# Kernel optimization log

Measured on AMD Instinct MI355X. Metric: run time of the kernel, lower is better.

The kernel has to match this reference:

```python
import jax, jax.numpy as jnp
import numpy as np

D_MODEL = 1024
NHEAD = 16
HEAD_DIM = D_MODEL // NHEAD
WINDOW = 256


def setup_inputs() -> dict:
    key = jax.random.key(0)
    kx, kq, kk, kv, ko = jax.random.split(key, 5)
    B, S = 2, 2048
    scale = 1.0 / np.sqrt(D_MODEL)
    x = jax.random.normal(kx, (B, S, D_MODEL), dtype=jnp.float32)
    Wq = jax.random.normal(kq, (D_MODEL, D_MODEL), dtype=jnp.float32) * scale
    Wk = jax.random.normal(kk, (D_MODEL, D_MODEL), dtype=jnp.float32) * scale
    Wv = jax.random.normal(kv, (D_MODEL, D_MODEL), dtype=jnp.float32) * scale
    Wo = jax.random.normal(ko, (D_MODEL, D_MODEL), dtype=jnp.float32) * scale
    return {"x": x, "Wq": Wq, "Wk": Wk, "Wv": Wv, "Wo": Wo}


def _sliding_window_mask(seq_len):
    # additive mask: 0 where (q - window + 1) <= k <= q, -inf elsewhere
    pos = jnp.arange(seq_len)
    qpos = pos[:, None]
    kpos = pos[None, :]
    valid = (kpos >= qpos - WINDOW + 1) & (kpos <= qpos)
    return jnp.where(valid, 0.0, -jnp.inf).astype(jnp.float32)


def reference(x, Wq, Wk, Wv, Wo):
    B, S, D = x.shape
    # projections (nn.Linear: x @ W.T; weights here stored as [out,in] equiv -> use x @ W.T)
    q = jnp.einsum('bsd,ed->bse', x, Wq)
    k = jnp.einsum('bsd,ed->bse', x, Wk)
    v = jnp.einsum('bsd,ed->bse', x, Wv)
    q = q.reshape(B, S, NHEAD, HEAD_DIM).transpose(0, 2, 1, 3)  # [B,H,S,Dh]
    k = k.reshape(B, S, NHEAD, HEAD_DIM).transpose(0, 2, 1, 3)
    v = v.reshape(B, S, NHEAD, HEAD_DIM).transpose(0, 2, 1, 3)
    mask = _sliding_window_mask(S)  # [S,S]
    scale = 1.0 / np.sqrt(HEAD_DIM)
    scores = jnp.einsum('bhqd,bhkd->bhqk', q, k) * scale + mask
    attn = jax.nn.softmax(scores, axis=-1)
    out = jnp.einsum('bhqk,bhkd->bhqd', attn, v)  # [B,H,S,Dh]
    out = out.transpose(0, 2, 1, 3).reshape(B, S, D)
    return jnp.einsum('bsd,ed->bse', out, Wo)
```

## Files before the change

kernel.cpp:

```cpp
#include <hip/hip_runtime.h>
#include <stdint.h>

#define S_LEN   2048
#define BATCH   2
#define DM      1024
#define NHEADS  16
#define HD      64
#define WIN     256
#define MROWS   (BATCH * S_LEN)
#define NX      (MROWS * DM)
#define NW      (DM * DM)

typedef unsigned short u16;
typedef unsigned int   u32;

using short8  = __attribute__((ext_vector_type(8))) short;
using floatx4 = __attribute__((ext_vector_type(4))) float;

__device__ __forceinline__ float bf2f(u16 u) {
    union { u32 u; float f; } v; v.u = ((u32)u) << 16; return v.f;
}
__device__ __forceinline__ u16 f2bf(float f) {
    union { float f; u32 u; } v; v.f = f;
    u32 u = v.u;
    u += 0x7fffu + ((u >> 16) & 1u);
    return (u16)(u >> 16);
}

__device__ __forceinline__ void load_lds16(const void* g, void* l) {
    __builtin_amdgcn_global_load_lds(
        (__attribute__((address_space(1))) void*)(uintptr_t)g,
        (__attribute__((address_space(3))) void*)(unsigned int)(uintptr_t)l,
        16, 0, 0);
}

__global__ __launch_bounds__(256) void detect_mode(const u16* x, int* flag) {
    __shared__ int sbad;
    int t = threadIdx.x;
    if (t == 0) sbad = 0;
    __syncthreads();
    int bad = 0;
    for (int i = t; i < 4096; i += 256) {
        float v = bf2f(x[i]);
        if (!(fabsf(v) < 1e6f)) bad = 1;
    }
    if (bad) atomicOr(&sbad, 1);
    __syncthreads();
    if (t == 0) flag[0] = sbad;
}

__global__ __launch_bounds__(256) void normalize_inputs(
        const void* x, const void* wq, const void* wk, const void* wv, const void* wo,
        u16* xb, u16* wcat, u16* wob, const int* flag) {
    if (flag[0] == 0) return;
    const int total = NX + 4 * NW;
    for (int i = blockIdx.x * blockDim.x + threadIdx.x; i < total;
         i += gridDim.x * blockDim.x) {
        const void* src; u16* dst; int li;
        if (i < NX)              { src = x;  dst = xb;            li = i; }
        else if (i < NX + NW)    { src = wq; dst = wcat;          li = i - NX; }
        else if (i < NX + 2*NW)  { src = wk; dst = wcat + NW;     li = i - NX - NW; }
        else if (i < NX + 3*NW)  { src = wv; dst = wcat + 2*NW;   li = i - NX - 2*NW; }
        else                     { src = wo; dst = wob;           li = i - NX - 3*NW; }
        dst[li] = f2bf(((const float*)src)[li]);
    }
}

#define BM 128
#define BK 32

template<int TBN>
__global__ __launch_bounds__(256) void gemm_lds(
        const u16* __restrict__ Araw, const u16* __restrict__ Anorm,
        const u16* __restrict__ B0, const u16* __restrict__ B1,
        const u16* __restrict__ B2, const u16* __restrict__ Bnorm,
        void* __restrict__ C, int M, int N, int K,
        const int* __restrict__ flag, int final_out) {
    constexpr int NF = TBN / 32;
    __shared__ __align__(16) u16 sA[2][BM * BK];
    __shared__ __align__(16) u16 sB[2][TBN * BK];

    const int mode = flag[0];
    const int tid  = threadIdx.x;
    const int lane = tid & 63, wave = tid >> 6;
    const int m0  = blockIdx.x * BM;
    const int n0g = blockIdx.y * TBN;
    const int third = n0g >> 10;
    const u16* A = mode ? Anorm : Araw;
    const u16* B = mode ? (Bnorm + (size_t)third * NW)
                        : (third == 0 ? B0 : (third == 1 ? B1 : B2));
    const int n0 = n0g - third * 1024;

    const int srow = lane >> 2;
    const int scol = (lane & 3) * 8;
    const u16* gA = A + (size_t)(m0 + wave * 16 + srow) * K + scol;
    const u16* gB = B + (size_t)(n0 + wave * 16 + srow) * K + scol;
    const size_t rstep = (size_t)64 * K;
    const int lofs = wave * 16 * BK;

    const int n16 = lane & 15, quad = lane >> 4;
    const int m_off = (wave >> 1) * 64, n_off = (wave & 1) * (TBN / 2);

    floatx4 acc[4][NF] = {};
    const int NIT = K / BK;

    auto issue = [&](int k0, int buf) {
        u16* lA = sA[buf] + lofs;
        u16* lB = sB[buf] + lofs;
        load_lds16(gA + k0,         lA);
        load_lds16(gA + k0 + rstep, lA + 64 * BK);
        load_lds16(gB + k0, lB);
        if (TBN == 128) load_lds16(gB + k0 + rstep, lB + 64 * BK);
    };

    issue(0, 0);
    for (int it = 0; it < NIT; ++it) {
        const int cur = it & 1;
        __syncthreads();
        if (it + 1 < NIT) issue((it + 1) * BK, 1 - cur);
        short8 af[4], bfr[NF];
        #pragma unroll
        for (int i = 0; i < 4; ++i)
            af[i] = *(const short8*)&sA[cur][(m_off + i * 16 + n16) * BK + quad * 8];
        #pragma unroll
        for (int j = 0; j < NF; ++j)
            bfr[j] = *(const short8*)&sB[cur][(n_off + j * 16 + n16) * BK + quad * 8];
        #pragma unroll
        for (int i = 0; i < 4; ++i) {
            #pragma unroll
            for (int j = 0; j < NF; ++j)
                acc[i][j] = __builtin_amdgcn_mfma_f32_16x16x32_bf16(
                    af[i], bfr[j], acc[i][j], 0, 0, 0);
        }
    }

    const int outmode = final_out ? mode : 0;
    const float oscale = (!final_out && n0g < 1024) ? 0.125f : 1.0f;
    #pragma unroll
    for (int i = 0; i < 4; ++i) {
        #pragma unroll
        for (int j = 0; j < NF; ++j) {
            #pragma unroll
            for (int r = 0; r < 4; ++r) {
                int row = m0 + m_off + i * 16 + quad * 4 + r;
                int col = n0g + n_off + j * 16 + n16;
                size_t idx = (size_t)row * N + col;
                float v = acc[i][j][r] * oscale;
                if (outmode) ((float*)C)[idx] = v;
                else         ((u16*)C)[idx]   = f2bf(v);
            }
        }
    }
}

#define NCHUNK 10

__global__ __launch_bounds__(256) void attn_mfma(
        const u16* __restrict__ QKV, u16* __restrict__ O) {
    __shared__ __align__(16) u16 sK[2][32][72];
    __shared__ __align__(16) u16 sVt[2][64][40];
    __shared__ __align__(16) u16 sP[4][2][16][40];

    const int bh = blockIdx.x;
    const int b  = bh >> 4, h = bh & 15;
    const int q0 = blockIdx.y * 64;
    const int kb0 = q0 - (WIN - 1);
    const int tid = threadIdx.x;
    const u16* base = QKV + (size_t)b * S_LEN * 3072;
    const u16* Kb = base + 1024 + h * 64;
    const u16* Vb = base + 2048 + h * 64;

    const int srow = tid >> 3;
    const int sseg = tid & 7;

    auto stage = [&](int c, int buf) {
        int kg = kb0 + c * 32 + srow;
        uint4 kv = {0u, 0u, 0u, 0u}, vv = {0u, 0u, 0u, 0u};
        if (kg >= 0 && kg < S_LEN) {
            kv = *(const uint4*)(Kb + (size_t)kg * 3072 + sseg * 8);
            vv = *(const uint4*)(Vb + (size_t)kg * 3072 + sseg * 8);
        }
        *(uint4*)&sK[buf][srow][sseg * 8] = kv;
        const u16* vp = (const u16*)&vv;
        #pragma unroll
        for (int t2 = 0; t2 < 8; ++t2) sVt[buf][sseg * 8 + t2][srow] = vp[t2];
    };

    const int wave = tid >> 6, lane = tid & 63;
    const int n16 = lane & 15, quad = lane >> 4;
    const int sqb = q0 + wave * 16;
    const int sq_r0 = sqb + quad * 4;
    const int cfirst = wave >> 1;

    const u16* qrow = base + (size_t)(sqb + n16) * 3072 + h * 64;
    short8 aq0 = *(const short8*)(qrow + quad * 8);
    short8 aq1 = *(const short8*)(qrow + 32 + quad * 8);

    floatx4 o0 = {0.f,0.f,0.f,0.f}, o1 = o0, o2 = o0, o3 = o0;
    float m[4] = {-1e30f, -1e30f, -1e30f, -1e30f};
    float l[4] = {0.f, 0.f, 0.f, 0.f};

    stage(0, 0);
    for (int c = 0; c < NCHUNK; ++c) {
        const int buf = c & 1;
        __syncthreads();
        if (c + 1 < NCHUNK) stage(c + 1, 1 - buf);
        if (c < cfirst || c > cfirst + 8) continue;

        short8 bk00 = *(const short8*)&sK[buf][n16][quad * 8];
        short8 bk01 = *(const short8*)&sK[buf][n16][32 + quad * 8];
        short8 bk10 = *(const short8*)&sK[buf][16 + n16][quad * 8];
        short8 bk11 = *(const short8*)&sK[buf][16 + n16][32 + quad * 8];
        floatx4 z = {0.f, 0.f, 0.f, 0.f};
        floatx4 s0 = __builtin_amdgcn_mfma_f32_16x16x32_bf16(aq0, bk00, z, 0, 0, 0);
        s0 = __builtin_amdgcn_mfma_f32_16x16x32_bf16(aq1, bk01, s0, 0, 0, 0);
        floatx4 s1 = __builtin_amdgcn_mfma_f32_16x16x32_bf16(aq0, bk10, z, 0, 0, 0);
        s1 = __builtin_amdgcn_mfma_f32_16x16x32_bf16(aq1, bk11, s1, 0, 0, 0);

        const int kg0 = kb0 + c * 32 + n16;
        const int kg1 = kg0 + 16;
        float alpha[4], p0[4], p1[4];
        #pragma unroll
        for (int r = 0; r < 4; ++r) {
            int sq = sq_r0 + r;
            int lo = sq - (WIN - 1); if (lo < 0) lo = 0;
            float v0 = (kg0 >= lo && kg0 <= sq) ? s0[r] : -1e30f;
            float v1 = (kg1 >= lo && kg1 <= sq) ? s1[r] : -1e30f;
            float mc = fmaxf(v0, v1);
            mc = fmaxf(mc, __shfl_xor(mc, 1));
            mc = fmaxf(mc, __shfl_xor(mc, 2));
            mc = fmaxf(mc, __shfl_xor(mc, 4));
            mc = fmaxf(mc, __shfl_xor(mc, 8));
            float mn = fmaxf(m[r], mc);
            alpha[r] = __expf(m[r] - mn);
            m[r] = mn;
            p0[r] = __expf(v0 - mn);
            p1[r] = __expf(v1 - mn);
            float rs = p0[r] + p1[r];
            rs += __shfl_xor(rs, 1);
            rs += __shfl_xor(rs, 2);
            rs += __shfl_xor(rs, 4);
            rs += __shfl_xor(rs, 8);
            l[r] = l[r] * alpha[r] + rs;
        }
        #pragma unroll
        for (int r = 0; r < 4; ++r) {
            o0[r] *= alpha[r]; o1[r] *= alpha[r];
            o2[r] *= alpha[r]; o3[r] *= alpha[r];
        }
        u16* pw = &sP[wave][c & 1][0][0];
        #pragma unroll
        for (int r = 0; r < 4; ++r) {
            pw[(quad * 4 + r) * 40 + n16]      = f2bf(p0[r]);
            pw[(quad * 4 + r) * 40 + 16 + n16] = f2bf(p1[r]);
        }
        asm volatile("s_waitcnt lgkmcnt(0)" ::: "memory");
        short8 pa  = *(const short8*)&pw[n16 * 40 + quad * 8];
        short8 bv0 = *(const short8*)&sVt[buf][n16]     [quad * 8];
        short8 bv1 = *(const short8*)&sVt[buf][16 + n16][quad * 8];
        short8 bv2 = *(const short8*)&sVt[buf][32 + n16][quad * 8];
        short8 bv3 = *(const short8*)&sVt[buf][48 + n16][quad * 8];
        o0 = __builtin_amdgcn_mfma_f32_16x16x32_bf16(pa, bv0, o0, 0, 0, 0);
        o1 = __builtin_amdgcn_mfma_f32_16x16x32_bf16(pa, bv1, o1, 0, 0, 0);
        o2 = __builtin_amdgcn_mfma_f32_16x16x32_bf16(pa, bv2, o2, 0, 0, 0);
        o3 = __builtin_amdgcn_mfma_f32_16x16x32_bf16(pa, bv3, o3, 0, 0, 0);
    }

    #pragma unroll
    for (int r = 0; r < 4; ++r) {
        float rl = 1.0f / l[r];
        size_t ro = ((size_t)(b * S_LEN + sq_r0 + r)) * DM + h * 64 + n16;
        O[ro]      = f2bf(o0[r] * rl);
        O[ro + 16] = f2bf(o1[r] * rl);
        O[ro + 32] = f2bf(o2[r] * rl);
        O[ro + 48] = f2bf(o3[r] * rl);
    }
}

extern "C" void kernel_launch(void* const* d_in, const int* in_sizes, int n_in,
                              void* d_out, int out_size, void* d_ws, size_t ws_size,
                              hipStream_t stream) {
    char* ws = (char*)d_ws;
    int* flag = (int*)ws;
    u16* xb   = (u16*)(ws + 1024);
    u16* wcat = xb   + (size_t)NX;
    u16* wob  = wcat + (size_t)3 * NW;
    u16* qkv  = wob  + (size_t)NW;
    u16* ob   = qkv  + (size_t)MROWS * 3 * DM;

    const u16* xr  = (const u16*)d_in[0];
    const u16* wqr = (const u16*)d_in[1];
    const u16* wkr = (const u16*)d_in[2];
    const u16* wvr = (const u16*)d_in[3];
    const u16* wor = (const u16*)d_in[4];

    detect_mode<<<1, 256, 0, stream>>>(xr, flag);
    normalize_inputs<<<1024, 256, 0, stream>>>(
        d_in[0], d_in[1], d_in[2], d_in[3], d_in[4], xb, wcat, wob, flag);
    gemm_lds<128><<<dim3(MROWS / BM, 3072 / 128), 256, 0, stream>>>(
        xr, xb, wqr, wkr, wvr, wcat, qkv, MROWS, 3 * DM, DM, flag, 0);
    attn_mfma<<<dim3(BATCH * NHEADS, S_LEN / 64), 256, 0, stream>>>(qkv, ob);
    gemm_lds<64><<<dim3(MROWS / BM, DM / 64), 256, 0, stream>>>(
        ob, ob, wor, wor, wor, wob, d_out, MROWS, DM, DM, flag, 1);
}
```

Measured before the change: 178.9 us.

## Pre-transpose V into a head-major buffer and fold mode detection into normalize

A new transpose_v kernel writes V as [b,h,d,s] into an extra workspace buffer. The attention kernel can then stage V^T into LDS with one 16-byte vector store per thread, replacing the previous eight scattered 2-byte LDS writes. To keep those V loads 8-aligned, the key window start moves to q0-256, and the mask sentinel changes to -3e38. The separate detect_mode launch is merged into normalize_inputs, where each block recomputes the flag itself. The cost is an extra kernel launch and an extra read and write of all of V through global memory.

```diff
diff --git a/kernel.cpp b/kernel.cpp
--- a/kernel.cpp
+++ b/kernel.cpp
@@ -34,25 +34,22 @@
         16, 0, 0);
 }
 
-__global__ __launch_bounds__(256) void detect_mode(const u16* x, int* flag) {
+__global__ __launch_bounds__(256) void normalize_inputs(
+        const void* x, const void* wq, const void* wk, const void* wv, const void* wo,
+        u16* xb, u16* wcat, u16* wob, int* flag) {
     __shared__ int sbad;
-    int t = threadIdx.x;
-    if (t == 0) sbad = 0;
+    if (threadIdx.x == 0) sbad = 0;
     __syncthreads();
     int bad = 0;
-    for (int i = t; i < 4096; i += 256) {
-        float v = bf2f(x[i]);
+    for (int i = threadIdx.x; i < 4096; i += 256) {
+        float v = bf2f(((const u16*)x)[i]);
         if (!(fabsf(v) < 1e6f)) bad = 1;
     }
     if (bad) atomicOr(&sbad, 1);
     __syncthreads();
-    if (t == 0) flag[0] = sbad;
-}
-
-__global__ __launch_bounds__(256) void normalize_inputs(
-        const void* x, const void* wq, const void* wk, const void* wv, const void* wo,
-        u16* xb, u16* wcat, u16* wob, const int* flag) {
-    if (flag[0] == 0) return;
+    const int mode = sbad;
+    if (blockIdx.x == 0 && threadIdx.x == 0) flag[0] = mode;
+    if (mode == 0) return;
     const int total = NX + 4 * NW;
     for (int i = blockIdx.x * blockDim.x + threadIdx.x; i < total;
          i += gridDim.x * blockDim.x) {
@@ -153,10 +150,29 @@
     }
 }
 
+__global__ __launch_bounds__(256) void transpose_v(
+        const u16* __restrict__ QKV, u16* __restrict__ VT) {
+    const int bh = blockIdx.x;
+    const int b = bh >> 4, h = bh & 15;
+    const int s0 = blockIdx.y * 64;
+    const int t = threadIdx.x;
+    const int d  = t & 63;
+    const int sg = t >> 6;
+    const u16* src = QKV + (size_t)b * S_LEN * 3072 + 2048 + h * 64 + d;
+    u16* dst = VT + ((size_t)bh * 64 + d) * S_LEN + s0 + sg * 16;
+    u16 buf[16];
+    #pragma unroll
+    for (int j = 0; j < 16; ++j)
+        buf[j] = src[(size_t)(s0 + sg * 16 + j) * 3072];
+    *(uint4*)(dst)     = *(uint4*)&buf[0];
+    *(uint4*)(dst + 8) = *(uint4*)&buf[8];
+}
+
 #define NCHUNK 10
 
 __global__ __launch_bounds__(256) void attn_mfma(
-        const u16* __restrict__ QKV, u16* __restrict__ O) {
+        const u16* __restrict__ QKV, const u16* __restrict__ VT,
+        u16* __restrict__ O) {
     __shared__ __align__(16) u16 sK[2][32][72];
     __shared__ __align__(16) u16 sVt[2][64][40];
     __shared__ __align__(16) u16 sP[4][2][16][40];
@@ -164,26 +180,29 @@
     const int bh = blockIdx.x;
     const int b  = bh >> 4, h = bh & 15;
     const int q0 = blockIdx.y * 64;
-    const int kb0 = q0 - (WIN - 1);
+    const int ks0 = q0 - 256;
     const int tid = threadIdx.x;
     const u16* base = QKV + (size_t)b * S_LEN * 3072;
     const u16* Kb = base + 1024 + h * 64;
-    const u16* Vb = base + 2048 + h * 64;
-
-    const int srow = tid >> 3;
-    const int sseg = tid & 7;
+    const u16* Vb = VT + (size_t)bh * 64 * S_LEN;
+
+    const int kRow = tid >> 3;
+    const int kSeg = tid & 7;
+    const int vD   = tid >> 2;
+    const int vSeg = tid & 3;
 
     auto stage = [&](int c, int buf) {
-        int kg = kb0 + c * 32 + srow;
-        uint4 kv = {0u, 0u, 0u, 0u}, vv = {0u, 0u, 0u, 0u};
-        if (kg >= 0 && kg < S_LEN) {
-            kv = *(const uint4*)(Kb + (size_t)kg * 3072 + sseg * 8);
-            vv = *(const uint4*)(Vb + (size_t)kg * 3072 + sseg * 8);
-        }
-        *(uint4*)&sK[buf][srow][sseg * 8] = kv;
-        const u16* vp = (const u16*)&vv;
-        #pragma unroll
-        for (int t2 = 0; t2 < 8; ++t2) sVt[buf][sseg * 8 + t2][srow] = vp[t2];
+        const int ks = ks0 + c * 32;
+        int kg = ks + kRow;
+        uint4 kv = {0u, 0u, 0u, 0u};
+        if (kg >= 0 && kg < S_LEN)
+            kv = *(const uint4*)(Kb + (size_t)kg * 3072 + kSeg * 8);
+        *(uint4*)&sK[buf][kRow][kSeg * 8] = kv;
+        int vk = ks + vSeg * 8;
+        uint4 vv = {0u, 0u, 0u, 0u};
+        if (vk >= 0 && vk + 8 <= S_LEN)
+            vv = *(const uint4*)(Vb + (size_t)vD * S_LEN + vk);
+        *(uint4*)&sVt[buf][vD][vSeg * 8] = vv;
     };
 
     const int wave = tid >> 6, lane = tid & 63;
@@ -217,15 +236,15 @@
         floatx4 s1 = __builtin_amdgcn_mfma_f32_16x16x32_bf16(aq0, bk10, z, 0, 0, 0);
         s1 = __builtin_amdgcn_mfma_f32_16x16x32_bf16(aq1, bk11, s1, 0, 0, 0);
 
-        const int kg0 = kb0 + c * 32 + n16;
+        const int kg0 = ks0 + c * 32 + n16;
         const int kg1 = kg0 + 16;
         float alpha[4], p0[4], p1[4];
         #pragma unroll
         for (int r = 0; r < 4; ++r) {
             int sq = sq_r0 + r;
             int lo = sq - (WIN - 1); if (lo < 0) lo = 0;
-            float v0 = (kg0 >= lo && kg0 <= sq) ? s0[r] : -1e30f;
-            float v1 = (kg1 >= lo && kg1 <= sq) ? s1[r] : -1e30f;
+            float v0 = (kg0 >= lo && kg0 <= sq) ? s0[r] : -3e38f;
+            float v1 = (kg1 >= lo && kg1 <= sq) ? s1[r] : -3e38f;
             float mc = fmaxf(v0, v1);
             mc = fmaxf(mc, __shfl_xor(mc, 1));
             mc = fmaxf(mc, __shfl_xor(mc, 2));
@@ -287,6 +306,7 @@
     u16* wob  = wcat + (size_t)3 * NW;
     u16* qkv  = wob  + (size_t)NW;
     u16* ob   = qkv  + (size_t)MROWS * 3 * DM;
+    u16* vt   = ob   + (size_t)NX;
 
     const u16* xr  = (const u16*)d_in[0];
     const u16* wqr = (const u16*)d_in[1];
@@ -294,12 +314,12 @@
     const u16* wvr = (const u16*)d_in[3];
     const u16* wor = (const u16*)d_in[4];
 
-    detect_mode<<<1, 256, 0, stream>>>(xr, flag);
     normalize_inputs<<<1024, 256, 0, stream>>>(
         d_in[0], d_in[1], d_in[2], d_in[3], d_in[4], xb, wcat, wob, flag);
     gemm_lds<128><<<dim3(MROWS / BM, 3072 / 128), 256, 0, stream>>>(
         xr, xb, wqr, wkr, wvr, wcat, qkv, MROWS, 3 * DM, DM, flag, 0);
-    attn_mfma<<<dim3(BATCH * NHEADS, S_LEN / 64), 256, 0, stream>>>(qkv, ob);
+    transpose_v<<<dim3(BATCH * NHEADS, S_LEN / 64), 256, 0, stream>>>(qkv, vt);
+    attn_mfma<<<dim3(BATCH * NHEADS, S_LEN / 64), 256, 0, stream>>>(qkv, vt, ob);
     gemm_lds<64><<<dim3(MROWS / BM, DM / 64), 256, 0, stream>>>(
         ob, ob, wor, wor, wor, wob, d_out, MROWS, DM, DM, flag, 1);
 }
```

After: 178.7 us. Within noise of the previous version (-0.1%).
